# Kernel tuning notes

Measured on AMD Instinct MI355X. Metric: run time of the kernel, lower is better.

Reference implementation:

```python
import jax, jax.numpy as jnp
import numpy as np

B = 2048      # batch
S = 256       # num_hist_features (attention seq len)
D = 128       # model_dim
NSC = 16      # num scalar features
L = 2         # num attention layers
HURST = 0.1   # cfg.H
LN_EPS = 1e-5


def _log_fractional_kernel():
    # (|t-s| + 1e-9)^(H - 1.5), row-normalized, then log(k + 1e-9)
    idx = jnp.arange(S, dtype=jnp.float32)
    td = jnp.abs(idx[:, None] - idx[None, :]) + 1e-9
    kern = td ** (HURST - 1.5)
    kern = kern / kern.sum(axis=-1, keepdims=True)
    return jnp.log(kern + 1e-9)  # [S, S]


def setup_inputs() -> dict:
    key = jax.random.key(0)
    ks = jax.random.split(key, 20)
    sc = 0.02
    inp = {
        "x": jax.random.normal(ks[0], (B, NSC + S), dtype=jnp.float32),
        "scalar_W": jax.random.normal(ks[1], (NSC, D), dtype=jnp.float32) * sc,
        "scalar_b": jnp.zeros((D,), jnp.float32),
        "hist_W": jax.random.normal(ks[2], (1, D), dtype=jnp.float32) * sc,
        "hist_b": jnp.zeros((D,), jnp.float32),
        "qW": jax.random.normal(ks[3], (L, D, D), dtype=jnp.float32) * sc,
        "qb": jnp.zeros((L, D), jnp.float32),
        "kW": jax.random.normal(ks[4], (L, D, D), dtype=jnp.float32) * sc,
        "kb": jnp.zeros((L, D), jnp.float32),
        "vW": jax.random.normal(ks[5], (L, D, D), dtype=jnp.float32) * sc,
        "vb": jnp.zeros((L, D), jnp.float32),
        "ln_g": jnp.ones((L, D), jnp.float32),
        "ln_b": jnp.zeros((L, D), jnp.float32),
        "h1_W": jax.random.normal(ks[6], (D * (S + 1), 128), dtype=jnp.float32) * sc,
        "h1_b": jnp.zeros((128,), jnp.float32),
        "h2_W": jax.random.normal(ks[7], (128, 64), dtype=jnp.float32) * sc,
        "h2_b": jnp.zeros((64,), jnp.float32),
        "h3_W": jax.random.normal(ks[8], (64, 1), dtype=jnp.float32) * sc,
        "h3_b": jnp.zeros((1,), jnp.float32),
    }
    return inp


def _layernorm(h, g, b):
    mu = h.mean(axis=-1, keepdims=True)
    var = ((h - mu) ** 2).mean(axis=-1, keepdims=True)
    return (h - mu) * jax.lax.rsqrt(var + LN_EPS) * g + b


def reference(x, scalar_W, scalar_b, hist_W, hist_b, qW, qb, kW, kb, vW, vb,
              ln_g, ln_b, h1_W, h1_b, h2_W, h2_b, h3_W, h3_b):
    log_kern = _log_fractional_kernel()  # [S, S]
    scalar_feats = x[:, :-S]             # [B, NSC]
    hist_feats = x[:, -S:, None]         # [B, S, 1]
    scalar_emb = scalar_feats @ scalar_W + scalar_b   # [B, D]
    h = hist_feats @ hist_W + hist_b                   # [B, S, D]
    inv_sqrt_d = 1.0 / np.sqrt(D).astype(np.float32)
    for i in range(L):
        q = h @ qW[i] + qb[i]
        k = h @ kW[i] + kb[i]
        v = h @ vW[i] + vb[i]
        scores = jnp.einsum('bsd,btd->bst', q, k) * inv_sqrt_d  # [B,S,S]
        attn = jax.nn.softmax(scores + log_kern, axis=-1)
        out = jnp.einsum('bst,btd->bsd', attn, v)
        h = _layernorm(h + out, ln_g[i], ln_b[i])
    combined = jnp.concatenate([scalar_emb[:, None, :], h], axis=1).reshape(x.shape[0], -1)
    z = jax.nn.relu(combined @ h1_W + h1_b)
    z = jax.nn.relu(z @ h2_W + h2_b)
    return z @ h3_W + h3_b  # [B, 1]
```

## Files before the change

kernel.cpp:

```cpp
#include <hip/hip_runtime.h>
#include <cstddef>


typedef unsigned short u16;
typedef unsigned int u32;
typedef short short8 __attribute__((ext_vector_type(8)));
typedef u32 u32x2 __attribute__((ext_vector_type(2)));
typedef float floatx16 __attribute__((ext_vector_type(16)));

__device__ __forceinline__ float b2f(u16 u){ return __uint_as_float(((u32)u) << 16); }
__device__ __forceinline__ u16 f2b(float f){
  u32 u = __float_as_uint(f);
  return (u16)((u + 0x7fffu + ((u >> 16) & 1u)) >> 16);
}
__device__ __forceinline__ float ldf(const u16* p, size_t i, int f32){
  float v = f32 ? ((const float*)p)[i] : b2f(p[i]);
  return __builtin_isfinite(v) ? v : 0.f;
}
__device__ __forceinline__ u32 pk2(float a, float b){
  return ((u32)f2b(b) << 16) | (u32)f2b(a);
}
__device__ __forceinline__ int swz(int row, int ch){ return (row << 8) | ((ch ^ (row & 15)) << 4); }
__device__ __forceinline__ floatx16 fz(){
  floatx16 z;
#pragma unroll
  for (int i = 0; i < 16; ++i) z[i] = 0.f;
  return z;
}
__device__ __forceinline__ floatx16 MF(short8 a, short8 b, floatx16 c){
  return __builtin_amdgcn_mfma_f32_32x32x16_bf16(a, b, c, 0, 0, 0);
}
__device__ __forceinline__ short8 frag_from(floatx16 cv, int half, int q5){
  int r0 = half * 8;
  u32 e01 = pk2(cv[r0 + 0], cv[r0 + 1]);
  u32 e23 = pk2(cv[r0 + 2], cv[r0 + 3]);
  u32 o01 = pk2(cv[r0 + 4], cv[r0 + 5]);
  u32 o23 = pk2(cv[r0 + 6], cv[r0 + 7]);
  u32 s0 = q5 ? e01 : o01;
  u32 s1 = q5 ? e23 : o23;
  u32 r0v = __shfl_xor(s0, 32);
  u32 r1v = __shfl_xor(s1, 32);
  union { u32 u[4]; short8 v; } un;
  un.u[0] = q5 ? r0v : e01;
  un.u[1] = q5 ? r1v : e23;
  un.u[2] = q5 ? o01 : r0v;
  un.u[3] = q5 ? o23 : r1v;
  return un.v;
}

__global__ __launch_bounds__(256) void k_detect(const u16* x, int* dflag){
  __shared__ int red[256];
  int t = threadIdx.x, cnt = 0;
  for (int i = t; i < 4096; i += 256){
    u16 v = x[2 * i];
    int e = (v >> 7) & 0xFF;
    if (e == 0xFF || e >= 0x90 || (e > 0 && e <= 0x20)) ++cnt;
  }
  red[t] = cnt;
  __syncthreads();
  for (int off = 128; off > 0; off >>= 1){
    if (t < off) red[t] += red[t + off];
    __syncthreads();
  }
  if (t == 0) dflag[0] = (red[0] > 1000) ? 1 : 0;
}


__global__ __launch_bounds__(128) void k_prepw(const u16* qW, const u16* kW, const u16* vW,
                                               const u16* qb, u16* Mrow, u16* vWT, float* uv,
                                               const int* dflag){
  int fl = dflag[0];
  int i = blockIdx.x >> 7, f = blockIdx.x & 127, e = threadIdx.x;
  size_t qo = (size_t)(i * 128 + e) * 128;
  size_t ko = (size_t)(i * 128 + f) * 128;
  float m = 0.f;
  for (int d = 0; d < 128; ++d) m += ldf(qW, qo + d, fl) * ldf(kW, ko + d, fl);
  const float RS = 0.08838834764831845f;
  Mrow[(i * 128 + e) * 128 + f] = f2b(m * RS);
  vWT[(i * 128 + f) * 128 + e] = f2b(ldf(vW, qo + f, fl));
  __shared__ float red[128];
  red[e] = ldf(kW, ko + e, fl) * ldf(qb, (size_t)i * 128 + e, fl);
  __syncthreads();
  for (int off = 64; off > 0; off >>= 1){
    if (e < off) red[e] += red[e + off];
    __syncthreads();
  }
  if (e == 0) uv[i * 128 + f] = red[0] * RS;
}

__global__ __launch_bounds__(256) void k_h1t(const u16* h1W, u16* h1WT, const int* dflag){
  int fl = dflag[0];
  __shared__ u16 tile[64][130];
  int k0 = blockIdx.x * 64, tid = threadIdx.x;
#pragma unroll 4
  for (int it = 0; it < 32; ++it){
    int r = it * 2 + (tid >> 7), c = tid & 127;
    tile[r][c] = f2b(ldf(h1W, (size_t)(k0 + r) * 128 + c, fl));
  }
  __syncthreads();
#pragma unroll 4
  for (int it = 0; it < 32; ++it){
    int idx = it * 256 + tid, n = idx >> 6, kk = idx & 63;
    h1WT[(size_t)n * 32896 + k0 + kk] = tile[kk][n];
  }
}


__global__ __launch_bounds__(512, 2) void k_fan(
    const u16* x, const u16* sW, const u16* sb, const u16* hW, const u16* hbe,
    const u16* Mrow, const float* uv, const u16* vWT, const u16* vb,
    const u16* lng, const u16* lnb,
    u16* hgq, u16* se, int qoff, const int* dflag){
  __shared__ alignas(16) u16 hL[32768];
  __shared__ alignas(16) u16 vt[16384];
  __shared__ alignas(16) u16 khL[16384];
  __shared__ float c_all[256];
  __shared__ float u_lds[128];
  int fl = dflag[0];
  int bl = blockIdx.x;
  int b = qoff + bl;
  int tid = threadIdx.x, w = tid >> 6, lane = tid & 63, l31 = lane & 31, q5 = lane >> 5;
  size_t xo = (size_t)b * 272;
  const float LKOFF = -20.72326584f;

  if (tid < 128){
    float acc = ldf(sb, tid, fl);
#pragma unroll
    for (int j = 0; j < 16; ++j) acc += ldf(x, xo + j, fl) * ldf(sW, (size_t)j * 128 + tid, fl);
    se[(size_t)b * 128 + tid] = f2b(acc);
  }
#pragma unroll
  for (int it = 0; it < 8; ++it){
    int c = it * 512 + tid, s = c >> 4, ch = c & 15;
    float xv = ldf(x, xo + 16 + s, fl);
    short8 r;
#pragma unroll
    for (int j = 0; j < 8; ++j)
      r[j] = (short)f2b(xv * ldf(hW, ch * 8 + j, fl) + ldf(hbe, ch * 8 + j, fl));
    *(short8*)((char*)hL + swz(s, ch)) = r;
  }

#pragma unroll 1
  for (int li = 0; li < 2; ++li){
    const u16* Mri  = Mrow + li * 16384;
    const u16* vWTi = vWT + li * 16384;
    if (tid < 128) u_lds[tid] = uv[li * 128 + tid];
    __syncthreads();

    {
      int row = 32 * w + l31;
      float dot = 0.f;
#pragma unroll 2
      for (int kc = 0; kc < 8; ++kc){
        int ch = 2 * kc + q5;
        short8 hv = *(const short8*)((char*)hL + swz(row, ch));
#pragma unroll
        for (int j = 0; j < 8; ++j) dot += u_lds[ch * 8 + j] * b2f(hv[j]);
      }
      dot += __shfl_xor(dot, 32);
      if (q5 == 0) c_all[row] = dot;
    }

    float ls_tot = 0.f;
    floatx16 oacc[4];
#pragma unroll
    for (int nt = 0; nt < 4; ++nt) oacc[nt] = fz();
    int scol = 32 * w + l31;

#pragma unroll 1
    for (int tt = 0; tt < 2; ++tt){
      int t0 = tt * 128;
      __syncthreads();
      int mtv = w & 3, ntv0 = (w >> 2) * 2;
      {
        const u16* Ma = Mri + (32 * mtv + l31) * 128 + q5 * 8;
#pragma unroll 1
        for (int j = 0; j < 2; ++j){
          int ntv = ntv0 + j;
          floatx16 ka = fz();
#pragma unroll 2
          for (int kc = 0; kc < 8; ++kc){
            short8 av = *(const short8*)(Ma + kc * 16);
            short8 bh = *(const short8*)((char*)hL + swz(t0 + 32 * ntv + l31, 2 * kc + q5));
            ka = MF(av, bh, ka);
          }
          int tloc = 32 * ntv + l31;
#pragma unroll
          for (int qd = 0; qd < 4; ++qd){
            u32x2 pv;
            pv.x = pk2(ka[4 * qd + 0], ka[4 * qd + 1]);
            pv.y = pk2(ka[4 * qd + 2], ka[4 * qd + 3]);
            *(u32x2*)((char*)khL + swz(tloc, 4 * mtv + qd) + 8 * q5) = pv;
          }
        }
      }
      {
        const u16* Va = vWTi + (32 * mtv + l31) * 128 + q5 * 8;
        float vbl = ldf(vb, (size_t)li * 128 + 32 * mtv + l31, fl);
#pragma unroll 1
        for (int j = 0; j < 2; ++j){
          int rj = t0 + 32 * (ntv0 + j) + l31;
          floatx16 va = fz();
#pragma unroll 2
          for (int kc = 0; kc < 8; ++kc){
            short8 avV = *(const short8*)(Va + kc * 16);
            short8 bh  = *(const short8*)((char*)hL + swz(rj, 2 * kc + q5));
            va = MF(bh, avV, va);
          }
#pragma unroll
          for (int qd = 0; qd < 4; ++qd){
            u32x2 pv;
            pv.x = pk2(va[4 * qd + 0] + vbl, va[4 * qd + 1] + vbl);
            pv.y = pk2(va[4 * qd + 2] + vbl, va[4 * qd + 3] + vbl);
            *(u32x2*)((char*)vt + swz(32 * mtv + l31, 4 * (ntv0 + j) + qd) + 8 * q5) = pv;
          }
        }
      }
      __syncthreads();
#pragma unroll 1
      for (int mt = 0; mt < 4; ++mt){
        floatx16 sa = fz();
        __builtin_amdgcn_s_setprio(1);
#pragma unroll 2
        for (int kc = 0; kc < 8; ++kc){
          short8 ak = *(const short8*)((char*)khL + swz(32 * mt + l31, 2 * kc + q5));
          short8 bq = *(const short8*)((char*)hL + swz(32 * w + l31, 2 * kc + q5));
          sa = MF(ak, bq, sa);
        }
        __builtin_amdgcn_s_setprio(0);
#pragma unroll
        for (int reg = 0; reg < 16; ++reg){
          int trl = 32 * mt + (reg & 3) + 8 * (reg >> 2) + 4 * q5;
          int tg = t0 + trl;
          float lk = (tg == scol) ? 0.f : LKOFF;
          float v = sa[reg] + c_all[tg] + lk;
          v = fminf(fmaxf(v, -50.f), 50.f);
          float p = __expf(v - 8.f);
          sa[reg] = p;
          ls_tot += p;
        }
        short8 pf0 = frag_from(sa, 0, q5);
        short8 pf1 = frag_from(sa, 1, q5);
        __builtin_amdgcn_s_setprio(1);
#pragma unroll
        for (int nt = 0; nt < 4; ++nt){
          short8 bv0 = *(const short8*)((char*)vt + swz(32 * nt + l31, 2 * (2 * mt + 0) + q5));
          oacc[nt] = MF(pf0, bv0, oacc[nt]);
          short8 bv1 = *(const short8*)((char*)vt + swz(32 * nt + l31, 2 * (2 * mt + 1) + q5));
          oacc[nt] = MF(pf1, bv1, oacc[nt]);
        }
        __builtin_amdgcn_s_setprio(0);
      }
    }
    __syncthreads();

    float l_run = ls_tot + __shfl_xor(ls_tot, 32);
    float linv = 1.f / l_run;
    float gv[4], bbv[4];
#pragma unroll
    for (int nt = 0; nt < 4; ++nt){
      gv[nt]  = ldf(lng, (size_t)li * 128 + 32 * nt + l31, fl);
      bbv[nt] = ldf(lnb, (size_t)li * 128 + 32 * nt + l31, fl);
    }
#pragma unroll
    for (int reg = 0; reg < 16; ++reg){
      int rr = (reg & 3) + 8 * (reg >> 2) + 4 * q5;
      int srow = 32 * w + rr;
      float lrv = __shfl(linv, rr);
      float s1 = 0.f, s2 = 0.f;
#pragma unroll
      for (int nt = 0; nt < 4; ++nt){
        int d = 32 * nt + l31;
        float res = b2f(*(const u16*)((char*)hL + swz(srow, d >> 3) + (d & 7) * 2));
        float v = oacc[nt][reg] * lrv + res;
        oacc[nt][reg] = v;
        s1 += v; s2 += v * v;
      }
#pragma unroll
      for (int off = 1; off < 32; off <<= 1){ s1 += __shfl_xor(s1, off); s2 += __shfl_xor(s2, off); }
      float mu = s1 * 0.0078125f;
      float rs = rsqrtf(fmaxf(s2 * 0.0078125f - mu * mu, 0.f) + 1e-5f);
#pragma unroll
      for (int nt = 0; nt < 4; ++nt){
        int d = 32 * nt + l31;
        float v = (oacc[nt][reg] - mu) * rs * gv[nt] + bbv[nt];
        *(u16*)((char*)hL + swz(srow, d >> 3) + (d & 7) * 2) = f2b(v);
      }
    }
    __syncthreads();
  }

#pragma unroll
  for (int it = 0; it < 8; ++it){
    int c = it * 512 + tid, row = c >> 4, ch = c & 15;
    *(short8*)(hgq + (size_t)bl * 32768 + row * 128 + ch * 8) =
        *(const short8*)((char*)hL + swz(row, ch));
  }
}


__global__ __launch_bounds__(256) void k_mlp1(const u16* se, const u16* hgq, const u16* h1WT,
                                              float* part, int qoff, int nb){
  int mb = blockIdx.x, ks = blockIdx.y;
  int tid = threadIdx.x, w = tid >> 6, lane = tid & 63, l31 = lane & 31, q5 = lane >> 5;
  int b0 = mb * 32;
  floatx16 acc = fz();
  const u16* brow = h1WT + (size_t)(32 * w + l31) * 32896;
  int br = b0 + l31;
  const u16* seb = se + (size_t)(qoff + br) * 128;
  const u16* hb = hgq + (size_t)br * 32768;
  for (int kk = 0; kk < 257; ++kk){
    int kbase = ks * 4112 + kk * 16;
    const u16* ap = (kbase < 128) ? (seb + kbase + q5 * 8) : (hb + (kbase - 128) + q5 * 8);
    short8 a = *(const short8*)ap;
    short8 bf = *(const short8*)(brow + kbase + q5 * 8);
    acc = MF(a, bf, acc);
  }
#pragma unroll
  for (int reg = 0; reg < 16; ++reg){
    int rr = (reg & 3) + 8 * (reg >> 2) + 4 * q5;
    part[(size_t)ks * nb * 128 + (size_t)(b0 + rr) * 128 + 32 * w + l31] = acc[reg];
  }
}

__global__ __launch_bounds__(256) void k_mlp1red(const float* part, const u16* h1b, float* z1q,
                                                 const int* dflag, int nb){
  int fl = dflag[0];
  int idx = blockIdx.x * 256 + threadIdx.x;
  float s = ldf(h1b, idx & 127, fl);
  size_t stride = (size_t)nb * 128;
#pragma unroll
  for (int ks = 0; ks < 8; ++ks) s += part[(size_t)ks * stride + idx];
  z1q[idx] = fmaxf(s, 0.f);
}

__global__ __launch_bounds__(256) void k_mlp2(const float* z1, const u16* h2W, const u16* h2b,
                                              float* z2, const int* dflag){
  int fl = dflag[0];
  int idx = blockIdx.x * 256 + threadIdx.x;
  int b = idx >> 6, j = idx & 63;
  float s = ldf(h2b, j, fl);
  const float* zr = z1 + (size_t)b * 128;
  for (int k = 0; k < 128; ++k) s += zr[k] * ldf(h2W, (size_t)k * 64 + j, fl);
  z2[idx] = fmaxf(s, 0.f);
}

__global__ __launch_bounds__(256) void k_mlp3(const float* z2, const u16* h3W, const u16* h3b,
                                              void* out, const int* dflag){
  int fl = dflag[0];
  int b = blockIdx.x * 256 + threadIdx.x;
  float s = ldf(h3b, 0, fl);
  const float* zr = z2 + (size_t)b * 64;
#pragma unroll
  for (int j = 0; j < 64; ++j) s += zr[j] * ldf(h3W, j, fl);
  if (!__builtin_isfinite(s)) s = 0.f;
  if (fl) ((float*)out)[b] = s;
  else    ((u16*)out)[b] = f2b(s);
}


extern "C" void kernel_launch(void* const* d_in, const int* in_sizes, int n_in,
                              void* d_out, int out_size, void* d_ws, size_t ws_size,
                              hipStream_t stream) {
  const u16* x   = (const u16*)d_in[0];
  const u16* sW  = (const u16*)d_in[1];
  const u16* sb  = (const u16*)d_in[2];
  const u16* hW  = (const u16*)d_in[3];
  const u16* hb  = (const u16*)d_in[4];
  const u16* qW  = (const u16*)d_in[5];
  const u16* qb  = (const u16*)d_in[6];
  const u16* kW  = (const u16*)d_in[7];
  const u16* vW  = (const u16*)d_in[9];
  const u16* vb  = (const u16*)d_in[10];
  const u16* lng = (const u16*)d_in[11];
  const u16* lnb = (const u16*)d_in[12];
  const u16* h1W = (const u16*)d_in[13];
  const u16* h1b = (const u16*)d_in[14];
  const u16* h2W = (const u16*)d_in[15];
  const u16* h2b = (const u16*)d_in[16];
  const u16* h3W = (const u16*)d_in[17];
  const u16* h3b = (const u16*)d_in[18];

  const int nb = (ws_size >= 153600000ull) ? 2048 : 512;
  const int nq = 2048 / nb;

  char* W = (char*)d_ws;
  size_t o = 0;
  u16*   hg    = (u16*)(W + o); o += (size_t)nb * 65536;
  u16*   h1WT  = (u16*)(W + o); o += 8421376;
  u16*   se    = (u16*)(W + o); o += 524288;
  u16*   Mrow  = (u16*)(W + o); o += 65536;
  u16*   vWT   = (u16*)(W + o); o += 65536;
  float* uv    = (float*)(W + o); o += 1024;
  float* part  = (float*)(W + o); o += (size_t)nb * 4096;
  float* z1    = (float*)(W + o); o += 1048576;
  float* z2    = (float*)(W + o); o += 524288;
  int*   dflag = (int*)(W + o);

  k_detect<<<1, 256, 0, stream>>>(x, dflag);
  k_prepw<<<256, 128, 0, stream>>>(qW, kW, vW, qb, Mrow, vWT, uv, dflag);
  k_h1t<<<514, 256, 0, stream>>>(h1W, h1WT, dflag);

  for (int q = 0; q < nq; ++q){
    int qoff = q * nb;
    k_fan<<<nb, 512, 0, stream>>>(x, sW, sb, hW, hb, Mrow, uv, vWT, vb,
                                  lng, lnb, hg, se, qoff, dflag);
    k_mlp1<<<dim3(nb / 32, 8), 256, 0, stream>>>(se, hg, h1WT, part, qoff, nb);
    k_mlp1red<<<nb / 2, 256, 0, stream>>>(part, h1b, z1 + (size_t)qoff * 128, dflag, nb);
  }

  k_mlp2<<<512, 256, 0, stream>>>(z1, h2W, h2b, z2, dflag);
  k_mlp3<<<8, 256, 0, stream>>>(z2, h3W, h3b, d_out, dflag);
}
```

Before: 1.053 ms.

## Double-buffer K/V projection tiles to overlap with attention compute

```diff
diff --git a/kernel.cpp b/kernel.cpp
--- a/kernel.cpp
+++ b/kernel.cpp
@@ -140,43 +140,29 @@
     *(short8*)((char*)hL + swz(s, ch)) = r;
   }
 
+  int mtv = w & 3, ntv = w >> 2;
+  int scol = 32 * w + l31;
+
 #pragma unroll 1
   for (int li = 0; li < 2; ++li){
     const u16* Mri  = Mrow + li * 16384;
     const u16* vWTi = vWT + li * 16384;
     if (tid < 128) u_lds[tid] = uv[li * 128 + tid];
+    float vbl = ldf(vb, (size_t)li * 128 + 32 * mtv + l31, fl);
     __syncthreads();
 
-    {
-      int row = 32 * w + l31;
-      float dot = 0.f;
-#pragma unroll 2
-      for (int kc = 0; kc < 8; ++kc){
-        int ch = 2 * kc + q5;
-        short8 hv = *(const short8*)((char*)hL + swz(row, ch));
-#pragma unroll
-        for (int j = 0; j < 8; ++j) dot += u_lds[ch * 8 + j] * b2f(hv[j]);
-      }
-      dot += __shfl_xor(dot, 32);
-      if (q5 == 0) c_all[row] = dot;
-    }
-
-    float ls_tot = 0.f;
+    float ls_a = 0.f, ls_b = 0.f;
     floatx16 oacc[4];
 #pragma unroll
     for (int nt = 0; nt < 4; ++nt) oacc[nt] = fz();
-    int scol = 32 * w + l31;
 
 #pragma unroll 1
-    for (int tt = 0; tt < 2; ++tt){
-      int t0 = tt * 128;
-      __syncthreads();
-      int mtv = w & 3, ntv0 = (w >> 2) * 2;
-      {
-        const u16* Ma = Mri + (32 * mtv + l31) * 128 + q5 * 8;
-#pragma unroll 1
-        for (int j = 0; j < 2; ++j){
-          int ntv = ntv0 + j;
+    for (int it = 0; it < 5; ++it){
+      if (it) __syncthreads();
+      if (it < 4){
+        int t0 = it * 64, buf = it & 1;
+        {
+          const u16* Ma = Mri + (32 * mtv + l31) * 128 + q5 * 8;
           floatx16 ka = fz();
 #pragma unroll 2
           for (int kc = 0; kc < 8; ++kc){
@@ -184,7 +170,7 @@
             short8 bh = *(const short8*)((char*)hL + swz(t0 + 32 * ntv + l31, 2 * kc + q5));
             ka = MF(av, bh, ka);
           }
-          int tloc = 32 * ntv + l31;
+          int tloc = 64 * buf + 32 * ntv + l31;
 #pragma unroll
           for (int qd = 0; qd < 4; ++qd){
             u32x2 pv;
@@ -193,18 +179,13 @@
             *(u32x2*)((char*)khL + swz(tloc, 4 * mtv + qd) + 8 * q5) = pv;
           }
         }
-      }
-      {
-        const u16* Va = vWTi + (32 * mtv + l31) * 128 + q5 * 8;
-        float vbl = ldf(vb, (size_t)li * 128 + 32 * mtv + l31, fl);
-#pragma unroll 1
-        for (int j = 0; j < 2; ++j){
-          int rj = t0 + 32 * (ntv0 + j) + l31;
+        {
+          const u16* Va = vWTi + (32 * mtv + l31) * 128 + q5 * 8;
           floatx16 va = fz();
 #pragma unroll 2
           for (int kc = 0; kc < 8; ++kc){
             short8 avV = *(const short8*)(Va + kc * 16);
-            short8 bh  = *(const short8*)((char*)hL + swz(rj, 2 * kc + q5));
+            short8 bh  = *(const short8*)((char*)hL + swz(t0 + 32 * ntv + l31, 2 * kc + q5));
             va = MF(bh, avV, va);
           }
 #pragma unroll
@@ -212,48 +193,63 @@
             u32x2 pv;
             pv.x = pk2(va[4 * qd + 0] + vbl, va[4 * qd + 1] + vbl);
             pv.y = pk2(va[4 * qd + 2] + vbl, va[4 * qd + 3] + vbl);
-            *(u32x2*)((char*)vt + swz(32 * mtv + l31, 4 * (ntv0 + j) + qd) + 8 * q5) = pv;
-          }
+            *(u32x2*)((char*)vt + swz(32 * mtv + l31, 8 * buf + 4 * ntv + qd) + 8 * q5) = pv;
+          }
+        }
+        if (it == 0){
+          int row = 32 * w + l31;
+          float dot = 0.f;
+#pragma unroll 2
+          for (int kc = 0; kc < 8; ++kc){
+            int ch = 2 * kc + q5;
+            short8 hv = *(const short8*)((char*)hL + swz(row, ch));
+#pragma unroll
+            for (int j = 0; j < 8; ++j) dot += u_lds[ch * 8 + j] * b2f(hv[j]);
+          }
+          dot += __shfl_xor(dot, 32);
+          if (q5 == 0) c_all[row] = dot;
         }
       }
-      __syncthreads();
+      if (it > 0){
+        int ti = it - 1, buf = ti & 1, t0g = ti * 64;
 #pragma unroll 1
-      for (int mt = 0; mt < 4; ++mt){
-        floatx16 sa = fz();
-        __builtin_amdgcn_s_setprio(1);
+        for (int mt = 0; mt < 2; ++mt){
+          floatx16 sa = fz();
+          __builtin_amdgcn_s_setprio(1);
 #pragma unroll 2
-        for (int kc = 0; kc < 8; ++kc){
-          short8 ak = *(const short8*)((char*)khL + swz(32 * mt + l31, 2 * kc + q5));
-          short8 bq = *(const short8*)((char*)hL + swz(32 * w + l31, 2 * kc + q5));
-          sa = MF(ak, bq, sa);
+          for (int kc = 0; kc < 8; ++kc){
+            short8 ak = *(const short8*)((char*)khL + swz(64 * buf + 32 * mt + l31, 2 * kc + q5));
+            short8 bq = *(const short8*)((char*)hL + swz(32 * w + l31, 2 * kc + q5));
+            sa = MF(ak, bq, sa);
+          }
+          __builtin_amdgcn_s_setprio(0);
+#pragma unroll
+          for (int reg = 0; reg < 16; ++reg){
+            int trl = 32 * mt + (reg & 3) + 8 * (reg >> 2) + 4 * q5;
+            int tg = t0g + trl;
+            float lk = (tg == scol) ? 0.f : LKOFF;
+            float v = sa[reg] + c_all[tg] + lk;
+            v = fminf(fmaxf(v, -50.f), 50.f);
+            float p = __expf(v - 8.f);
+            sa[reg] = p;
+            if (reg & 1) ls_b += p; else ls_a += p;
+          }
+          short8 pf0 = frag_from(sa, 0, q5);
+          short8 pf1 = frag_from(sa, 1, q5);
+          __builtin_amdgcn_s_setprio(1);
+#pragma unroll
+          for (int nt = 0; nt < 4; ++nt){
+            short8 bv0 = *(const short8*)((char*)vt + swz(32 * nt + l31, 8 * buf + 2 * (2 * mt + 0) + q5));
+            oacc[nt] = MF(pf0, bv0, oacc[nt]);
+            short8 bv1 = *(const short8*)((char*)vt + swz(32 * nt + l31, 8 * buf + 2 * (2 * mt + 1) + q5));
+            oacc[nt] = MF(pf1, bv1, oacc[nt]);
+          }
+          __builtin_amdgcn_s_setprio(0);
         }
-        __builtin_amdgcn_s_setprio(0);
-#pragma unroll
-        for (int reg = 0; reg < 16; ++reg){
-          int trl = 32 * mt + (reg & 3) + 8 * (reg >> 2) + 4 * q5;
-          int tg = t0 + trl;
-          float lk = (tg == scol) ? 0.f : LKOFF;
-          float v = sa[reg] + c_all[tg] + lk;
-          v = fminf(fmaxf(v, -50.f), 50.f);
-          float p = __expf(v - 8.f);
-          sa[reg] = p;
-          ls_tot += p;
-        }
-        short8 pf0 = frag_from(sa, 0, q5);
-        short8 pf1 = frag_from(sa, 1, q5);
-        __builtin_amdgcn_s_setprio(1);
-#pragma unroll
-        for (int nt = 0; nt < 4; ++nt){
-          short8 bv0 = *(const short8*)((char*)vt + swz(32 * nt + l31, 2 * (2 * mt + 0) + q5));
-          oacc[nt] = MF(pf0, bv0, oacc[nt]);
-          short8 bv1 = *(const short8*)((char*)vt + swz(32 * nt + l31, 2 * (2 * mt + 1) + q5));
-          oacc[nt] = MF(pf1, bv1, oacc[nt]);
-        }
-        __builtin_amdgcn_s_setprio(0);
       }
     }
-    __syncthreads();
-
+
+    float ls_tot = ls_a + ls_b;
     float l_run = ls_tot + __shfl_xor(ls_tot, 32);
     float linv = 1.f / l_run;
     float gv[4], bbv[4];
```

After: 1.189 ms. 1.13x slower.
